# Optimization experiments

Measured on AMD Instinct MI355X. Metric: run time of the kernel, lower is better.

Reference implementation:

```python
import math
import jax, jax.numpy as jnp
import numpy as np

N_HEADS = 16
D_HEAD = 128
D_ROPE = 64  # d_head // 2
ROPE_SCALE = 40.0


def _rotate_half(x):
    x1, x2 = jnp.split(x, 2, axis=-1)
    return jnp.concatenate([-x2, x1], axis=-1)


def _apply_rotary(x, cos, sin):
    # rotate only the first cos.shape[-1] dims of the rope slice
    half = cos.shape[-1]
    x_rot, x_base = x[..., :half], x[..., half:]
    x_rot = x_rot * cos + _rotate_half(x_rot) * sin
    return jnp.concatenate([x_rot, x_base], axis=-1)


def _forward(x, W_dkv, W_dq, W_uk, W_uv, W_uq, W_kr, W_qr, W_out):
    B, S, H = x.shape
    c_kv = x @ W_dkv                                   # [B,S,cd]
    c_q = x @ W_dq                                     # [B,S,cd]
    q_c = c_q @ W_uq                                   # [B,S,up]
    k_c = c_kv @ W_uk                                  # [B,S,up]
    v = (c_kv @ W_uv).reshape(B, S, N_HEADS, D_HEAD)   # [B,S,h,d]
    k_r = (x @ W_kr).reshape(B, S, N_HEADS, D_ROPE)
    q_r = (q_c @ W_qr).reshape(B, S, N_HEADS, D_ROPE)

    # RoPE (partial: first d_rope//2 dims rotated, rest passthrough)
    half_dim = D_ROPE // 2
    inv_freq = 1.0 / (10000.0 ** (jnp.arange(0, half_dim, 2, dtype=jnp.float32) / half_dim))
    t = jnp.arange(S, dtype=jnp.float32) / ROPE_SCALE
    freqs = jnp.einsum('i,j->ij', t, inv_freq)         # [S, d_rope//4]
    rotation = jnp.concatenate([freqs, freqs], axis=-1)  # [S, d_rope//2]
    cos = jnp.cos(rotation)[None, :, None, :]
    sin = jnp.sin(rotation)[None, :, None, :]
    k_rope = _apply_rotary(k_r, cos, sin)
    q_rope = _apply_rotary(q_r, cos, sin)

    k = jnp.concatenate([k_c.reshape(B, S, N_HEADS, D_HEAD - D_ROPE), k_rope], axis=-1)
    q = jnp.concatenate([q_c.reshape(B, S, N_HEADS, D_HEAD - D_ROPE), q_rope], axis=-1)

    # NOTE: faithful to source: einsum takes (k, q) in that order, and the
    # softmax result is computed but UNUSED (AV uses raw scores). Replicated.
    scores = jnp.einsum('bihd,bjhd->bhij', k, q) / math.sqrt(D_HEAD)
    out = jnp.einsum('bhij,bjhd->bihd', scores, v)     # [B,S,h,d]
    output = out.reshape(B, S, N_HEADS * D_HEAD) @ W_out
    return output, c_kv, k_rope


def setup_inputs() -> dict:
    key = jax.random.key(0)
    ks = jax.random.split(key, 9)
    B, S, H, CD, UP = 2, 2048, 2048, 1024, 1024
    w = lambda k, shp: jax.random.normal(k, shp, dtype=jnp.float32) * 0.02
    return {
        'x': jax.random.normal(ks[0], (B, S, H), dtype=jnp.float32),
        'W_dkv': w(ks[1], (H, CD)),
        'W_dq': w(ks[2], (H, CD)),
        'W_uk': w(ks[3], (CD, UP)),
        'W_uv': w(ks[4], (CD, N_HEADS * D_HEAD)),
        'W_uq': w(ks[5], (CD, UP)),
        'W_kr': w(ks[6], (H, N_HEADS * D_ROPE)),
        'W_qr': w(ks[7], (CD, N_HEADS * D_ROPE)),
        'W_out': w(ks[8], (N_HEADS * D_HEAD, H)),
    }


def reference(x, W_dkv, W_dq, W_uk, W_uv, W_uq, W_kr, W_qr, W_out):
    return _forward(x, W_dkv, W_dq, W_uk, W_uv, W_uq, W_kr, W_qr, W_out)
```

## Files before the change

kernel.cpp:

```cpp
#include <hip/hip_runtime.h>
#include <math.h>

typedef _Float16 half8 __attribute__((ext_vector_type(8)));
typedef float floatx4 __attribute__((ext_vector_type(4)));

typedef const uint32_t __attribute__((address_space(1)))* gp1_t;
typedef uint32_t __attribute__((address_space(3)))* lp3_t;
#define GLDS16(g, l) __builtin_amdgcn_global_load_lds((gp1_t)(const void*)(g), (lp3_t)(void*)(l), 16, 0, 0)

#define BK 32

__global__ __launch_bounds__(256) void gemm_fast(
    const _Float16* __restrict__ A, const _Float16* __restrict__ B,
    float* __restrict__ Cf, _Float16* __restrict__ Ch,
    float* __restrict__ Cx, _Float16* __restrict__ Cy,
    int Kc, long lda, long ldb, long ldcf, long ldch,
    int cmap, long cf_lo, long cf_hi, float alpha, int nh, int nsk, int epi_mode,
    long aoff_b, long aoff_h, long boff_b, long boff_h,
    long coff_b, long coff_h, long coff_s)
{
    __shared__ __align__(16) _Float16 As[128 * BK];
    __shared__ __align__(16) _Float16 Bs[128 * BK];

    const int z = blockIdx.z;
    const int hs = nh * nsk;
    const int zb = z / hs;
    const int rr = z % hs;
    const int zh = rr / nsk;
    const int ks = rr % nsk;

    const _Float16* Ab = A + (long)zb * aoff_b + (long)zh * aoff_h + (long)ks * Kc;
    const _Float16* Bb = B + (long)zb * boff_b + (long)zh * boff_h + (long)ks * Kc;
    const long cofs = (long)zb * coff_b + (long)zh * coff_h + (long)ks * coff_s;

    const long m0 = (long)blockIdx.y * 128;
    const long n0 = (long)blockIdx.x * 128;
    const int t = threadIdx.x;
    const int wave = t >> 6, lane = t & 63;
    const int lr = lane & 15, lq = lane >> 4;
    const int wm = (wave & 1) * 64, wn = (wave >> 1) * 64;

    const int c0 = wave * 64 + lane;
    const int c1 = c0 + 256;
    const _Float16* ga0 = Ab + (m0 + (c0 >> 2)) * lda + (c0 & 3) * 8;
    const _Float16* ga1 = Ab + (m0 + (c1 >> 2)) * lda + (c1 & 3) * 8;
    const _Float16* gb0 = Bb + (n0 + (c0 >> 2)) * ldb + (c0 & 3) * 8;
    const _Float16* gb1 = Bb + (n0 + (c1 >> 2)) * ldb + (c1 & 3) * 8;
    _Float16* lA0 = As + wave * 512;
    _Float16* lA1 = As + 2048 + wave * 512;
    _Float16* lB0 = Bs + wave * 512;
    _Float16* lB1 = Bs + 2048 + wave * 512;

    floatx4 acc[4][4];
    #pragma unroll
    for (int i = 0; i < 4; ++i)
        #pragma unroll
        for (int j = 0; j < 4; ++j) acc[i][j] = (floatx4){0.f, 0.f, 0.f, 0.f};

    for (int k0 = 0; k0 < Kc; k0 += BK) {
        GLDS16(ga0, lA0); GLDS16(ga1, lA1);
        GLDS16(gb0, lB0); GLDS16(gb1, lB1);
        ga0 += BK; ga1 += BK; gb0 += BK; gb1 += BK;
        __syncthreads();

        half8 a[4], b[4];
        #pragma unroll
        for (int i = 0; i < 4; ++i) a[i] = *(const half8*)(As + (wm + i * 16 + lr) * BK + lq * 8);
        #pragma unroll
        for (int j = 0; j < 4; ++j) b[j] = *(const half8*)(Bs + (wn + j * 16 + lr) * BK + lq * 8);
        #pragma unroll
        for (int i = 0; i < 4; ++i)
            #pragma unroll
            for (int j = 0; j < 4; ++j)
                acc[i][j] = __builtin_amdgcn_mfma_f32_16x16x32_f16(a[i], b[j], acc[i][j], 0, 0, 0);
        __syncthreads();
    }

    if (epi_mode == 0) {
        #pragma unroll
        for (int i = 0; i < 4; ++i)
            #pragma unroll
            for (int j = 0; j < 4; ++j)
                #pragma unroll
                for (int r = 0; r < 4; ++r) {
                    long row = m0 + wm + i * 16 + lq * 4 + r;
                    long col = n0 + wn + j * 16 + lr;
                    float v = alpha * acc[i][j][r];
                    if (Ch) {
                        long cm = cmap ? ((col >> 6) * 128 + (col & 63)) : col;
                        Ch[cofs + row * ldch + cm] = (_Float16)v;
                    }
                    if (Cf && col >= cf_lo && col < cf_hi)
                        Cf[cofs + row * ldcf + (col - cf_lo)] = v;
                }
    } else if (epi_mode == 1) {
        const int nb = (int)n0 + wn;
        if (nb < 2048) {
            #pragma unroll
            for (int i = 0; i < 4; ++i)
                #pragma unroll
                for (int j = 0; j < 4; ++j)
                    #pragma unroll
                    for (int r = 0; r < 4; ++r) {
                        long row = m0 + wm + i * 16 + lq * 4 + r;
                        long col = n0 + wn + j * 16 + lr;
                        float v = acc[i][j][r];
                        Ch[row * 2048 + col] = (_Float16)v;
                        if (nb < 1024) Cf[row * 1024 + col] = v;
                    }
        } else {
            const int h = (nb - 2048) >> 6;
            const float invf = powf(10000.0f, -(float)lr / 16.0f);
            #pragma unroll
            for (int i = 0; i < 4; ++i)
                #pragma unroll
                for (int r = 0; r < 4; ++r) {
                    long row = m0 + wm + i * 16 + lq * 4 + r;
                    int s = (int)row & 2047;
                    float ang = ((float)s / 40.0f) * invf;
                    float cv = cosf(ang), sv = sinf(ang);
                    float v0 = acc[i][0][r], v1 = acc[i][1][r];
                    float y[4] = { v0 * cv - v1 * sv, v1 * cv + v0 * sv,
                                   acc[i][2][r], acc[i][3][r] };
                    #pragma unroll
                    for (int j = 0; j < 4; ++j) {
                        int d = j * 16 + lr;
                        Cx[row * 1024 + h * 64 + d] = y[j];
                        Cy[row * 2048 + h * 128 + 64 + d] = (_Float16)y[j];
                    }
                }
        }
    } else {
        if (zb == 0) {
            #pragma unroll
            for (int i = 0; i < 4; ++i)
                #pragma unroll
                for (int j = 0; j < 4; ++j)
                    #pragma unroll
                    for (int r = 0; r < 4; ++r) {
                        long row = m0 + wm + i * 16 + lq * 4 + r;
                        long col = n0 + wn + j * 16 + lr;
                        Ch[cofs + row * ldch + col] = (_Float16)acc[i][j][r];
                    }
        } else {
            const int mb = (int)m0 + wm;
            if (mb < 1024) {
                #pragma unroll
                for (int i = 0; i < 4; ++i)
                    #pragma unroll
                    for (int j = 0; j < 4; ++j)
                        #pragma unroll
                        for (int r = 0; r < 4; ++r) {
                            long u = m0 + wm + i * 16 + lq * 4 + r;
                            long col = n0 + wn + j * 16 + lr;
                            long qrow = ((u >> 6) << 7) + (u & 63);
                            Ch[cofs + qrow * 4096 + col] = (_Float16)acc[i][j][r];
                        }
            } else {
                const int h = (mb - 1024) >> 6;
                const float invf = powf(10000.0f, -(float)(lq * 4) / 16.0f);
                #pragma unroll
                for (int j = 0; j < 4; ++j)
                    #pragma unroll
                    for (int r = 0; r < 4; ++r) {
                        long col = n0 + wn + j * 16 + lr;
                        int s = (int)col & 2047;
                        int j16 = lq * 4 + r;
                        float ivf = powf(10000.0f, -(float)j16 / 16.0f);
                        float ang = ((float)s / 40.0f) * ivf;
                        float cv = cosf(ang), sv = sinf(ang);
                        float v0 = acc[0][j][r], v1 = acc[1][j][r];
                        float y[4] = { v0 * cv - v1 * sv, v1 * cv + v0 * sv,
                                       acc[2][j][r], acc[3][j][r] };
                        #pragma unroll
                        for (int i = 0; i < 4; ++i) {
                            int dd = i * 16 + lq * 4 + r;
                            long qrow = h * 128 + 64 + dd;
                            Ch[cofs + qrow * 4096 + col] = (_Float16)y[i];
                        }
                    }
                (void)invf;
            }
        }
    }
}

__device__ inline void tr_tile(const float* __restrict__ in, _Float16* __restrict__ out,
                               int R, int C, int tile, int tx, int ty, float (*tb)[33])
{
    int tc = tile % (C >> 5), tr = tile / (C >> 5);
    int c0 = tc * 32, r0 = tr * 32;
    for (int i = ty; i < 32; i += 8)
        tb[i][tx] = in[(long)(r0 + i) * C + c0 + tx];
    __syncthreads();
    for (int i = ty; i < 32; i += 8)
        out[(long)(c0 + i) * R + r0 + tx] = (_Float16)tb[tx][i];
}

__device__ inline void cast_blk(const float* __restrict__ in, _Float16* __restrict__ out,
                                int blk, int tid)
{
    long idx = (long)blk * 2048 + tid * 8;
    float4 a = ((const float4*)(in + idx))[0];
    float4 b = ((const float4*)(in + idx))[1];
    half8 h = { (_Float16)a.x, (_Float16)a.y, (_Float16)a.z, (_Float16)a.w,
                (_Float16)b.x, (_Float16)b.y, (_Float16)b.z, (_Float16)b.w };
    *(half8*)(out + idx) = h;
}

__global__ void prep_kernel(
    const float* __restrict__ x, const float* __restrict__ W_dkv,
    const float* __restrict__ W_dq, const float* __restrict__ W_uk,
    const float* __restrict__ W_uv, const float* __restrict__ W_uq,
    const float* __restrict__ W_kr, const float* __restrict__ W_qr,
    const float* __restrict__ W_out,
    _Float16* __restrict__ WcatT, _Float16* __restrict__ WukT,
    _Float16* __restrict__ WuvT, _Float16* __restrict__ WuqcatT,
    _Float16* __restrict__ WqrT, _Float16* __restrict__ Wuqh,
    _Float16* __restrict__ WoutT, _Float16* __restrict__ xh)
{
    __shared__ float tb[32][33];
    int blk = blockIdx.x;
    int tid = threadIdx.x;
    int tx = tid & 31, ty = tid >> 5;
    if (blk < 2048)        tr_tile(W_dkv, WcatT,            2048, 1024, blk,         tx, ty, tb);
    else if (blk < 4096)   tr_tile(W_dq,  WcatT + 2097152,  2048, 1024, blk - 2048,  tx, ty, tb);
    else if (blk < 6144)   tr_tile(W_kr,  WcatT + 4194304,  2048, 1024, blk - 4096,  tx, ty, tb);
    else if (blk < 7168)   tr_tile(W_uk,  WukT,             1024, 1024, blk - 6144,  tx, ty, tb);
    else if (blk < 8192)   tr_tile(W_uq,  WuqcatT,          1024, 1024, blk - 7168,  tx, ty, tb);
    else if (blk < 9216)   tr_tile(W_qr,  WqrT,             1024, 1024, blk - 8192,  tx, ty, tb);
    else if (blk < 11264)  tr_tile(W_uv,  WuvT,             1024, 2048, blk - 9216,  tx, ty, tb);
    else if (blk < 15360)  tr_tile(W_out, WoutT,            2048, 2048, blk - 11264, tx, ty, tb);
    else if (blk < 19456)  cast_blk(x,    xh,   blk - 15360, tid);
    else                   cast_blk(W_uq, Wuqh, blk - 19456, tid);
}

__global__ void reduce8_cast_kernel(const float* __restrict__ in, _Float16* __restrict__ out)
{
    int i = blockIdx.x * 256 + threadIdx.x;
    float s = 0.f;
    #pragma unroll
    for (int j = 0; j < 8; ++j) s += in[i + j * 524288];
    out[i] = (_Float16)s;
}

extern "C" void kernel_launch(void* const* d_in, const int* in_sizes, int n_in,
                              void* d_out, int out_size, void* d_ws, size_t ws_size,
                              hipStream_t stream)
{
    const float* x     = (const float*)d_in[0];
    const float* W_dkv = (const float*)d_in[1];
    const float* W_dq  = (const float*)d_in[2];
    const float* W_uk  = (const float*)d_in[3];
    const float* W_uv  = (const float*)d_in[4];
    const float* W_uq  = (const float*)d_in[5];
    const float* W_kr  = (const float*)d_in[6];
    const float* W_qr  = (const float*)d_in[7];
    const float* W_out = (const float*)d_in[8];

    float* out_main  = (float*)d_out;
    float* out_ckv   = out_main + 8388608;
    float* out_krope = out_ckv + 4194304;

    char* w = (char*)d_ws;
    size_t off = 0;
    auto alloc = [&](size_t bytes) { void* p = w + off; off += (bytes + 255) & ~(size_t)255; return p; };

    _Float16* catA    = (_Float16*)alloc(16777216);
    _Float16* WcatT   = (_Float16*)alloc(12582912);
    _Float16* WukT    = (_Float16*)alloc(2097152);
    _Float16* WuvT    = (_Float16*)alloc(4194304);
    _Float16* WuqcatT = (_Float16*)alloc(4194304);
    _Float16* WqrT    = (_Float16*)alloc(2097152);
    _Float16* Wuqh    = (_Float16*)alloc(2097152);
    _Float16* WoutT   = (_Float16*)alloc(8388608);
    void*     reg_xm  = alloc(16777216);
    _Float16* k_flat  = (_Float16*)alloc(16777216);
    _Float16* vT      = (_Float16*)alloc(16777216);
    _Float16* qT      = (_Float16*)alloc(16777216);

    _Float16* xh      = (_Float16*)reg_xm;
    float*    Mbuf32p = (float*)reg_xm;
    _Float16* PT      = catA;
    _Float16* WuqrT   = WuqcatT + 1048576;
    _Float16* Mbuf16  = WukT;

    #define GF(A_,B_,Cf_,Ch_,Cx_,Cy_,M_,N_,Kc_,lda_,ldb_,ldcf_,ldch_,cmap_,cflo_,cfhi_,alpha_,nb_,nh_,nsk_,mode_,ab,ah,bb,bh,cb,ch2,cs) \
        hipLaunchKernelGGL(gemm_fast, dim3((N_)/128,(M_)/128,(nb_)*(nh_)*(nsk_)), dim3(256), 0, stream, \
            A_, B_, Cf_, Ch_, Cx_, Cy_, (int)(Kc_), (long)(lda_), (long)(ldb_), (long)(ldcf_), (long)(ldch_), \
            cmap_, (long)(cflo_), (long)(cfhi_), (float)(alpha_), nh_, nsk_, mode_, \
            (long)(ab),(long)(ah),(long)(bb),(long)(bh),(long)(cb),(long)(ch2),(long)(cs))

    hipLaunchKernelGGL(prep_kernel, dim3(19968), dim3(256), 0, stream,
        x, W_dkv, W_dq, W_uk, W_uv, W_uq, W_kr, W_qr, W_out,
        WcatT, WukT, WuvT, WuqcatT, WqrT, Wuqh, WoutT, xh);

    GF(xh, WcatT, out_ckv, catA, out_krope, k_flat, 4096, 3072, 2048, 2048, 2048, 0, 0,
       0, 0, 0, 1.0, 1, 1, 1, 1, 0,0,0,0,0,0,0);
    GF(WqrT, Wuqh, (float*)nullptr, WuqrT, (float*)nullptr, (_Float16*)nullptr,
       1024, 1024, 1024, 1024, 1024, 0, 1024, 0, 0, 0, 1.0, 1, 1, 1, 0, 0,0,0,0,0,0,0);
    GF(catA, WukT, (float*)nullptr, k_flat, (float*)nullptr, (_Float16*)nullptr,
       4096, 1024, 1024, 2048, 1024, 0, 2048, 1, 0, 0, 1.0, 1, 1, 1, 0, 0,0,0,0,0,0,0);
    GF(WuvT, catA, (float*)nullptr, vT, (float*)nullptr, (_Float16*)nullptr,
       2048, 4096, 1024, 1024, 2048, 0, 4096, 0, 0, 0, 1.0, 2, 1, 1, 2,
       2097152, 0, 1024, 0, 8388608, 0, 0);
    GF(qT, vT, Mbuf32p, (_Float16*)nullptr, (float*)nullptr, (_Float16*)nullptr,
       128, 128, 256, 4096, 4096, 128, 0, 0, 0, 128, 0.08838834764831845, 2, 16, 8, 0,
       2048, 524288, 2048, 524288, 262144, 16384, 524288);
    hipLaunchKernelGGL(reduce8_cast_kernel, dim3(2048), dim3(256), 0, stream, Mbuf32p, Mbuf16);
    GF(WoutT, Mbuf16, (float*)nullptr, PT, (float*)nullptr, (_Float16*)nullptr,
       2048, 128, 128, 2048, 128, 0, 2048, 0, 0, 0, 1.0, 2, 16, 1, 0,
       0, 128, 262144, 16384, 4194304, 128, 0);
    GF(k_flat, PT, out_main, (_Float16*)nullptr, (float*)nullptr, (_Float16*)nullptr,
       2048, 2048, 2048, 2048, 2048, 2048, 0, 0, 0, 2048, 1.0, 2, 1, 1, 0,
       4194304, 0, 4194304, 0, 4194304, 0, 0);

    #undef GF
}
```

Baseline: 474.9 us.

## Add 256x256-tile 8-wave pipelined GEMM kernel for the three largest GEMMs

Introduces a new GEMM kernel with 256x256 output tiles, 512 threads, 64-wide K steps double-buffered in 128 KB LDS via direct global-to-LDS loads, interleaved with MFMA phases using explicit barriers, waitcnt and setprio. The large projection, V-up and final attention-output GEMMs switch to it to raise arithmetic intensity and overlap loads with compute. Epilogues are ported, including the fused RoPE paths. Risks include low occupancy from heavy LDS and register use, and fewer blocks on some GEMM shapes.

```diff
diff --git a/kernel.cpp b/kernel.cpp
--- a/kernel.cpp
+++ b/kernel.cpp
@@ -9,6 +9,10 @@
 #define GLDS16(g, l) __builtin_amdgcn_global_load_lds((gp1_t)(const void*)(g), (lp3_t)(void*)(l), 16, 0, 0)
 
 #define BK 32
+
+#define BARRIER() __builtin_amdgcn_s_barrier()
+#define LGKM0()   asm volatile("s_waitcnt lgkmcnt(0)" ::: "memory")
+#define VM8()     asm volatile("s_waitcnt vmcnt(8)" ::: "memory")
 
 __global__ __launch_bounds__(256) void gemm_fast(
     const _Float16* __restrict__ A, const _Float16* __restrict__ B,
@@ -158,7 +162,6 @@
                         }
             } else {
                 const int h = (mb - 1024) >> 6;
-                const float invf = powf(10000.0f, -(float)(lq * 4) / 16.0f);
                 #pragma unroll
                 for (int j = 0; j < 4; ++j)
                     #pragma unroll
@@ -179,7 +182,215 @@
                             Ch[cofs + qrow * 4096 + col] = (_Float16)y[i];
                         }
                     }
-                (void)invf;
+            }
+        }
+    }
+}
+
+__global__ __launch_bounds__(512, 2) void gemm256(
+    const _Float16* __restrict__ A, const _Float16* __restrict__ B,
+    float* __restrict__ Cf, _Float16* __restrict__ Ch,
+    float* __restrict__ Cx, _Float16* __restrict__ Cy,
+    int Kc, long lda, long ldb, long ldcf, long ldch,
+    int cmap, long cf_lo, long cf_hi, float alpha, int nh, int nsk, int epi_mode,
+    long aoff_b, long aoff_h, long boff_b, long boff_h,
+    long coff_b, long coff_h, long coff_s)
+{
+    __shared__ __align__(16) _Float16 sm[65536];
+
+    const int z = blockIdx.z;
+    const int hs = nh * nsk;
+    const int zb = z / hs;
+    const int rr = z % hs;
+    const int zh = rr / nsk;
+    const int ks = rr % nsk;
+
+    const _Float16* Ab = A + (long)zb * aoff_b + (long)zh * aoff_h + (long)ks * Kc;
+    const _Float16* Bb = B + (long)zb * boff_b + (long)zh * boff_h + (long)ks * Kc;
+    const long cofs = (long)zb * coff_b + (long)zh * coff_h + (long)ks * coff_s;
+
+    const long m0 = (long)blockIdx.y * 256;
+    const long n0 = (long)blockIdx.x * 256;
+    const int t = threadIdx.x;
+    const int wave = t >> 6, lane = t & 63;
+    const int lr = lane & 15, lq = lane >> 4;
+    const int wm = (wave >> 2) * 128, wn = (wave & 3) * 64;
+    const int wmrb = wm >> 4, wnrb = wn >> 4;
+    const int NT = Kc >> 6;
+
+    floatx4 acc[8][4];
+    #pragma unroll
+    for (int i = 0; i < 8; ++i)
+        #pragma unroll
+        for (int j = 0; j < 4; ++j) acc[i][j] = (floatx4){0.f, 0.f, 0.f, 0.f};
+
+#define ST(tt_, kk_, q_, b_) do { \
+        const int tcl_ = (tt_) < NT ? (tt_) : (tt_) - NT; \
+        const int isB_ = (q_) >> 1; \
+        const int rb_ = ((q_) & 1) * 8 + wave; \
+        const long grow_ = (isB_ ? n0 : m0) + rb_ * 16 + lr; \
+        const _Float16* src_ = (isB_ ? Bb + grow_ * ldb : Ab + grow_ * lda) \
+                               + (long)tcl_ * 64 + (kk_) * 32 + lq * 8; \
+        _Float16* dst_ = sm + (b_) * 32768 + isB_ * 16384 + (rb_ * 2 + (kk_)) * 512; \
+        GLDS16(src_, dst_); \
+    } while (0)
+
+#define LOADA(ihb_, kk_) { _Pragma("unroll") \
+    for (int i_ = 0; i_ < 4; ++i_) \
+        aF[i_] = *(const half8*)(At + (((wmrb + (ihb_) + i_) * 2 + (kk_)) << 9) + lane * 8); }
+#define LOADB(kk_) { _Pragma("unroll") \
+    for (int j_ = 0; j_ < 4; ++j_) \
+        bF[j_] = *(const half8*)(Bt + (((wnrb + j_) * 2 + (kk_)) << 9) + lane * 8); }
+#define MFMA16(ihb_) { _Pragma("unroll") \
+    for (int i_ = 0; i_ < 4; ++i_) { _Pragma("unroll") \
+        for (int j_ = 0; j_ < 4; ++j_) \
+            acc[(ihb_) + i_][j_] = __builtin_amdgcn_mfma_f32_16x16x32_f16(aF[i_], bF[j_], acc[(ihb_) + i_][j_], 0, 0, 0); } }
+
+    ST(0, 0, 0, 0); ST(0, 0, 1, 0); ST(0, 0, 2, 0); ST(0, 0, 3, 0);
+    ST(0, 1, 0, 0); ST(0, 1, 1, 0); ST(0, 1, 2, 0); ST(0, 1, 3, 0);
+    ST(1, 0, 0, 1); ST(1, 0, 1, 1); ST(1, 0, 2, 1); ST(1, 0, 3, 1);
+    VM8(); BARRIER();
+
+    half8 aF[4], bF[4];
+    for (int tt = 0; tt < NT; ++tt) {
+        const int buf = tt & 1, ob = buf ^ 1;
+        const _Float16* At = sm + buf * 32768;
+        const _Float16* Bt = At + 16384;
+
+        LOADA(0, 0); LOADB(0);
+        ST(tt + 1, 1, 0, ob); ST(tt + 1, 1, 1, ob);
+        BARRIER(); LGKM0();
+        __builtin_amdgcn_s_setprio(1); MFMA16(0); __builtin_amdgcn_s_setprio(0);
+        BARRIER();
+        LOADA(4, 0);
+        ST(tt + 1, 1, 2, ob); ST(tt + 1, 1, 3, ob);
+        BARRIER(); LGKM0();
+        __builtin_amdgcn_s_setprio(1); MFMA16(4); __builtin_amdgcn_s_setprio(0);
+        VM8();
+        BARRIER();
+        LOADA(0, 1); LOADB(1);
+        ST(tt + 2, 0, 0, buf); ST(tt + 2, 0, 1, buf);
+        BARRIER(); LGKM0();
+        __builtin_amdgcn_s_setprio(1); MFMA16(0); __builtin_amdgcn_s_setprio(0);
+        BARRIER();
+        LOADA(4, 1);
+        ST(tt + 2, 0, 2, buf); ST(tt + 2, 0, 3, buf);
+        BARRIER(); LGKM0();
+        __builtin_amdgcn_s_setprio(1); MFMA16(4); __builtin_amdgcn_s_setprio(0);
+        VM8();
+        BARRIER();
+    }
+#undef ST
+#undef LOADA
+#undef LOADB
+#undef MFMA16
+
+    if (epi_mode == 0) {
+        #pragma unroll
+        for (int i = 0; i < 8; ++i)
+            #pragma unroll
+            for (int j = 0; j < 4; ++j)
+                #pragma unroll
+                for (int r = 0; r < 4; ++r) {
+                    long row = m0 + wm + i * 16 + lq * 4 + r;
+                    long col = n0 + wn + j * 16 + lr;
+                    float v = alpha * acc[i][j][r];
+                    if (Ch) {
+                        long cm = cmap ? ((col >> 6) * 128 + (col & 63)) : col;
+                        Ch[cofs + row * ldch + cm] = (_Float16)v;
+                    }
+                    if (Cf && col >= cf_lo && col < cf_hi)
+                        Cf[cofs + row * ldcf + (col - cf_lo)] = v;
+                }
+    } else if (epi_mode == 1) {
+        const int nb = (int)n0 + wn;
+        if (nb < 2048) {
+            #pragma unroll
+            for (int i = 0; i < 8; ++i)
+                #pragma unroll
+                for (int j = 0; j < 4; ++j)
+                    #pragma unroll
+                    for (int r = 0; r < 4; ++r) {
+                        long row = m0 + wm + i * 16 + lq * 4 + r;
+                        long col = n0 + wn + j * 16 + lr;
+                        float v = acc[i][j][r];
+                        Ch[row * 2048 + col] = (_Float16)v;
+                        if (nb < 1024) Cf[row * 1024 + col] = v;
+                    }
+        } else {
+            const int h = (nb - 2048) >> 6;
+            const float invf = powf(10000.0f, -(float)lr / 16.0f);
+            #pragma unroll
+            for (int i = 0; i < 8; ++i)
+                #pragma unroll
+                for (int r = 0; r < 4; ++r) {
+                    long row = m0 + wm + i * 16 + lq * 4 + r;
+                    int s = (int)row & 2047;
+                    float ang = ((float)s / 40.0f) * invf;
+                    float cv = cosf(ang), sv = sinf(ang);
+                    float v0 = acc[i][0][r], v1 = acc[i][1][r];
+                    float y[4] = { v0 * cv - v1 * sv, v1 * cv + v0 * sv,
+                                   acc[i][2][r], acc[i][3][r] };
+                    #pragma unroll
+                    for (int j = 0; j < 4; ++j) {
+                        int d = j * 16 + lr;
+                        Cx[row * 1024 + h * 64 + d] = y[j];
+                        Cy[row * 2048 + h * 128 + 64 + d] = (_Float16)y[j];
+                    }
+                }
+        }
+    } else {
+        if (zb == 0) {
+            #pragma unroll
+            for (int i = 0; i < 8; ++i)
+                #pragma unroll
+                for (int j = 0; j < 4; ++j)
+                    #pragma unroll
+                    for (int r = 0; r < 4; ++r) {
+                        long row = m0 + wm + i * 16 + lq * 4 + r;
+                        long col = n0 + wn + j * 16 + lr;
+                        Ch[cofs + row * ldch + col] = (_Float16)acc[i][j][r];
+                    }
+        } else {
+            const int mb = (int)m0 + wm;
+            if (mb < 1024) {
+                #pragma unroll
+                for (int i = 0; i < 8; ++i)
+                    #pragma unroll
+                    for (int j = 0; j < 4; ++j)
+                        #pragma unroll
+                        for (int r = 0; r < 4; ++r) {
+                            long u = m0 + wm + i * 16 + lq * 4 + r;
+                            long col = n0 + wn + j * 16 + lr;
+                            long qrow = ((u >> 6) << 7) + (u & 63);
+                            Ch[cofs + qrow * 4096 + col] = (_Float16)acc[i][j][r];
+                        }
+            } else {
+                const int hbase = (mb - 1024) >> 6;
+                #pragma unroll
+                for (int ih = 0; ih < 2; ++ih) {
+                    const int h = hbase + ih;
+                    #pragma unroll
+                    for (int j = 0; j < 4; ++j)
+                        #pragma unroll
+                        for (int r = 0; r < 4; ++r) {
+                            long col = n0 + wn + j * 16 + lr;
+                            int s = (int)col & 2047;
+                            int j16 = lq * 4 + r;
+                            float ivf = powf(10000.0f, -(float)j16 / 16.0f);
+                            float ang = ((float)s / 40.0f) * ivf;
+                            float cv = cosf(ang), sv = sinf(ang);
+                            float v0 = acc[ih * 4 + 0][j][r], v1 = acc[ih * 4 + 1][j][r];
+                            float y[4] = { v0 * cv - v1 * sv, v1 * cv + v0 * sv,
+                                           acc[ih * 4 + 2][j][r], acc[ih * 4 + 3][j][r] };
+                            #pragma unroll
+                            for (int ii = 0; ii < 4; ++ii) {
+                                int dd = ii * 16 + lq * 4 + r;
+                                long qrow = h * 128 + 64 + dd;
+                                Ch[cofs + qrow * 4096 + col] = (_Float16)y[ii];
+                            }
+                        }
+                }
             }
         }
     }
@@ -291,17 +502,23 @@
             cmap_, (long)(cflo_), (long)(cfhi_), (float)(alpha_), nh_, nsk_, mode_, \
             (long)(ab),(long)(ah),(long)(bb),(long)(bh),(long)(cb),(long)(ch2),(long)(cs))
 
+    #define GF256(A_,B_,Cf_,Ch_,Cx_,Cy_,M_,N_,Kc_,lda_,ldb_,ldcf_,ldch_,cmap_,cflo_,cfhi_,alpha_,nb_,nh_,nsk_,mode_,ab,ah,bb,bh,cb,ch2,cs) \
+        hipLaunchKernelGGL(gemm256, dim3((N_)/256,(M_)/256,(nb_)*(nh_)*(nsk_)), dim3(512), 0, stream, \
+            A_, B_, Cf_, Ch_, Cx_, Cy_, (int)(Kc_), (long)(lda_), (long)(ldb_), (long)(ldcf_), (long)(ldch_), \
+            cmap_, (long)(cflo_), (long)(cfhi_), (float)(alpha_), nh_, nsk_, mode_, \
+            (long)(ab),(long)(ah),(long)(bb),(long)(bh),(long)(cb),(long)(ch2),(long)(cs))
+
     hipLaunchKernelGGL(prep_kernel, dim3(19968), dim3(256), 0, stream,
         x, W_dkv, W_dq, W_uk, W_uv, W_uq, W_kr, W_qr, W_out,
         WcatT, WukT, WuvT, WuqcatT, WqrT, Wuqh, WoutT, xh);
 
-    GF(xh, WcatT, out_ckv, catA, out_krope, k_flat, 4096, 3072, 2048, 2048, 2048, 0, 0,
+    GF256(xh, WcatT, out_ckv, catA, out_krope, k_flat, 4096, 3072, 2048, 2048, 2048, 0, 0,
        0, 0, 0, 1.0, 1, 1, 1, 1, 0,0,0,0,0,0,0);
     GF(WqrT, Wuqh, (float*)nullptr, WuqrT, (float*)nullptr, (_Float16*)nullptr,
        1024, 1024, 1024, 1024, 1024, 0, 1024, 0, 0, 0, 1.0, 1, 1, 1, 0, 0,0,0,0,0,0,0);
     GF(catA, WukT, (float*)nullptr, k_flat, (float*)nullptr, (_Float16*)nullptr,
        4096, 1024, 1024, 2048, 1024, 0, 2048, 1, 0, 0, 1.0, 1, 1, 1, 0, 0,0,0,0,0,0,0);
-    GF(WuvT, catA, (float*)nullptr, vT, (float*)nullptr, (_Float16*)nullptr,
+    GF256(WuvT, catA, (float*)nullptr, vT, (float*)nullptr, (_Float16*)nullptr,
        2048, 4096, 1024, 1024, 2048, 0, 4096, 0, 0, 0, 1.0, 2, 1, 1, 2,
        2097152, 0, 1024, 0, 8388608, 0, 0);
     GF(qT, vT, Mbuf32p, (_Float16*)nullptr, (float*)nullptr, (_Float16*)nullptr,
@@ -311,9 +528,10 @@
     GF(WoutT, Mbuf16, (float*)nullptr, PT, (float*)nullptr, (_Float16*)nullptr,
        2048, 128, 128, 2048, 128, 0, 2048, 0, 0, 0, 1.0, 2, 16, 1, 0,
        0, 128, 262144, 16384, 4194304, 128, 0);
-    GF(k_flat, PT, out_main, (_Float16*)nullptr, (float*)nullptr, (_Float16*)nullptr,
+    GF256(k_flat, PT, out_main, (_Float16*)nullptr, (float*)nullptr, (_Float16*)nullptr,
        2048, 2048, 2048, 2048, 2048, 2048, 0, 0, 0, 2048, 1.0, 2, 1, 1, 0,
        4194304, 0, 4194304, 0, 4194304, 0, 0);
 
     #undef GF
-}
+    #undef GF256
+}
```

Measured after the change: 493.3 us. 3.9% more time.
